# Performance work log

Hardware: AMD Instinct MI355X
Metric: run time of the kernel (lower is better)

The kernel has to match this reference:

```python
import jax, jax.numpy as jnp
import numpy as np

B, F_IN, HID, H, S = 256, 1024, 1024, 16, 128
TEMP = float((HID // H) ** 0.5)  # 8.0


def setup_inputs() -> dict:
    key = jax.random.key(0)
    ks = jax.random.split(key, 7)
    return {
        "x": jax.random.normal(ks[0], (B, F_IN, S), dtype=jnp.float32),
        "Wq": jax.random.normal(ks[1], (HID, F_IN), dtype=jnp.float32) * (1.0 / np.sqrt(F_IN)),
        "bq": jax.random.normal(ks[2], (HID,), dtype=jnp.float32) * 0.01,
        "Wk": jax.random.normal(ks[3], (HID, F_IN), dtype=jnp.float32) * (1.0 / np.sqrt(F_IN)),
        "bk": jax.random.normal(ks[4], (HID,), dtype=jnp.float32) * 0.01,
        "Wo": jax.random.normal(ks[5], (S,), dtype=jnp.float32) * (1.0 / np.sqrt(S)),
        "bo": jax.random.normal(ks[6], (1,), dtype=jnp.float32) * 0.01,
    }


def _to_heads(t):
    # (B, F, S) -> (B, H, S, F//H), matching reshape(B,H,F/H,S).permute(0,1,3,2)
    b, f, s = t.shape
    return t.reshape(b, H, f // H, s).transpose(0, 1, 3, 2)


def reference(x, Wq, bq, Wk, bk, Wo, bo):
    # 1x1 Conv1d == per-position linear over channel dim
    q = jnp.einsum('bis,hi->bhs', x, Wq) + bq[None, :, None]
    k = jnp.einsum('bis,hi->bhs', x, Wk) + bk[None, :, None]
    qh = _to_heads(q)          # (B,H,S,HID/H)
    kh = _to_heads(k)          # (B,H,S,HID/H)
    vh = _to_heads(x)          # (B,H,S,F_IN/H)  -- v is the raw input, unprojected
    scores = jnp.einsum('bhsd,bhtd->bhst', qh, kh) / TEMP
    attn = jax.nn.softmax(scores, axis=-1)
    out = jnp.einsum('bhst,bhtd->bhsd', attn, vh)   # (B,H,S,F_IN/H)
    # _reshape_from_batches: (B,H,S,dv) -> (B, F_IN, S)
    out = out.transpose(0, 1, 3, 2).reshape(x.shape[0], F_IN, S)
    # map_o: Linear(num_users, 1) over last axis, then squeeze
    score = jnp.einsum('bfs,s->bf', out, Wo) + bo[0]
    return score
```

## Files before the change

kernel.cpp:

```cpp
#include <hip/hip_runtime.h>

#define F 1024
#define S 128
#define H 16
#define D 64
#define CK 64
#define NCHUNK 16

typedef short bf16x8 __attribute__((ext_vector_type(8)));
typedef float f32x4  __attribute__((ext_vector_type(4)));

#define XS_UNITS ((size_t)256 * NCHUNK * 1024)
#define WB_UNITS ((size_t)16 * NCHUNK * 1024)
#define WS_NEED ((XS_UNITS + WB_UNITS) * 16)

struct SmemT {
    uint4 mat[2048];
    float wpart[4][S];
    float wfin[S];
};

__device__ __forceinline__ unsigned short f2bf(float f) {
    unsigned u = __float_as_uint(f);
    u += 0x7fffu + ((u >> 16) & 1u);
    return (unsigned short)(u >> 16);
}

__device__ __forceinline__ uint4 pack8(const float* f) {
    uint4 u;
    u.x = (unsigned)f2bf(f[0]) | ((unsigned)f2bf(f[1]) << 16);
    u.y = (unsigned)f2bf(f[2]) | ((unsigned)f2bf(f[3]) << 16);
    u.z = (unsigned)f2bf(f[4]) | ((unsigned)f2bf(f[5]) << 16);
    u.w = (unsigned)f2bf(f[6]) | ((unsigned)f2bf(f[7]) << 16);
    return u;
}

typedef __attribute__((address_space(1))) const unsigned int as1_u32;
typedef __attribute__((address_space(3))) unsigned int as3_u32;

__device__ __forceinline__ void async_cp16(const uint4* g, uint4* l) {
    __builtin_amdgcn_global_load_lds((as1_u32*)g, (as3_u32*)l, 16, 0, 0);
}

__global__ void prep(const float* __restrict__ x,
                     const float* __restrict__ Wq,
                     const float* __restrict__ Wk,
                     uint4* __restrict__ xs,
                     uint4* __restrict__ wb)
{
    __shared__ float tile[64 * 129];
    const int tid = threadIdx.x;
    const int blk = blockIdx.x;
    if (blk < 4096) {
        const int b = blk >> 4, ch = blk & 15;
        const float4* src = (const float4*)(x + ((size_t)b * F + ch * CK) * S);
        float4 v[8];
#pragma unroll
        for (int j = 0; j < 8; ++j) v[j] = src[tid + j * 256];
#pragma unroll
        for (int j = 0; j < 8; ++j) {
            const int e4 = tid + j * 256;
            const int i  = e4 >> 5;
            const int sc = (e4 & 31) * 4;
            tile[i * 129 + sc + 0] = v[j].x;
            tile[i * 129 + sc + 1] = v[j].y;
            tile[i * 129 + sc + 2] = v[j].z;
            tile[i * 129 + sc + 3] = v[j].w;
        }
        __syncthreads();
#pragma unroll
        for (int j = 0; j < 4; ++j) {
            const int u   = tid + j * 256;
            const int s   = u >> 3;
            const int kc  = (u & 7) ^ (s & 7);
            float f[8];
#pragma unroll
            for (int jj = 0; jj < 8; ++jj) f[jj] = tile[(kc * 8 + jj) * 129 + s];
            xs[((size_t)(b * NCHUNK + ch)) * 1024 + u] = pack8(f);
        }
    } else {
        const int blk2 = blk - 4096;
        const int h = blk2 >> 4, ch = blk2 & 15;
#pragma unroll
        for (int j = 0; j < 4; ++j) {
            const int u   = tid + j * 256;
            const int row = u >> 3;
            const int kc  = (u & 7) ^ (row & 7);
            const float* src = (row < 64)
                ? (Wq + (size_t)(h * D + row) * F + ch * CK + kc * 8)
                : (Wk + (size_t)(h * D + row - 64) * F + ch * CK + kc * 8);
            float f[8];
            float4 a = ((const float4*)src)[0];
            float4 c = ((const float4*)src)[1];
            f[0] = a.x; f[1] = a.y; f[2] = a.z; f[3] = a.w;
            f[4] = c.x; f[5] = c.y; f[6] = c.z; f[7] = c.w;
            wb[((size_t)(h * NCHUNK + ch)) * 1024 + u] = pack8(f);
        }
    }
}

__launch_bounds__(256, 4)
__global__ void attn_main(const float* __restrict__ x,
                          const uint4* __restrict__ xs,
                          const uint4* __restrict__ wb,
                          const float* __restrict__ bq,
                          const float* __restrict__ bk,
                          const float* __restrict__ Wo,
                          const float* __restrict__ bo,
                          float* __restrict__ out)
{
    __shared__ SmemT sm;
    const int tid  = threadIdx.x;
    const int lane = tid & 63;
    const int wv   = tid >> 6;
    const int l15  = lane & 15;
    const int q    = lane >> 4;

    const int g    = blockIdx.x;
    const int xcd  = g & 7;
    const int slot = g >> 3;
    const int hg   = slot >> 7;
    const int r0   = slot & 127;
    const int b    = xcd * 32 + (r0 >> 2);
    const int h    = hg * 4 + (r0 & 3);

    const float* xb = x + (size_t)b * (F * S);
    const uint4* xc = xs + ((size_t)b * NCHUNK) * 1024;
    const uint4* wc = wb + ((size_t)h * NCHUNK) * 1024;

    const int m0 = (wv & 1) * 64;
    const int n0 = (wv >> 1) * 64;

    f32x4 acc[4][4];
#pragma unroll
    for (int mt = 0; mt < 4; ++mt)
#pragma unroll
        for (int nt = 0; nt < 4; ++nt) acc[mt][nt] = (f32x4){0.f, 0.f, 0.f, 0.f};

    for (int ch = 0; ch < NCHUNK; ++ch) {
        __syncthreads();
        const uint4* wg = wc + ch * 1024 + wv * 256;
        const uint4* xg = xc + ch * 1024 + wv * 256;
#pragma unroll
        for (int k = 0; k < 4; ++k)
            async_cp16(wg + k * 64 + lane, &sm.mat[wv * 256 + k * 64]);
#pragma unroll
        for (int k = 0; k < 4; ++k)
            async_cp16(xg + k * 64 + lane, &sm.mat[1024 + wv * 256 + k * 64]);
        __syncthreads();
#pragma unroll
        for (int ks = 0; ks < 2; ++ks) {
            bf16x8 af[4], br[4];
#pragma unroll
            for (int mt = 0; mt < 4; ++mt) {
                const int row = m0 + mt * 16 + l15;
                af[mt] = *(const bf16x8*)&sm.mat[row * 8 + ((ks * 4 + q) ^ (row & 7))];
            }
#pragma unroll
            for (int nt = 0; nt < 4; ++nt) {
                const int row = n0 + nt * 16 + l15;
                br[nt] = *(const bf16x8*)&sm.mat[1024 + row * 8 + ((ks * 4 + q) ^ (row & 7))];
            }
#pragma unroll
            for (int mt = 0; mt < 4; ++mt)
#pragma unroll
                for (int nt = 0; nt < 4; ++nt)
                    acc[mt][nt] = __builtin_amdgcn_mfma_f32_16x16x32_bf16(
                        af[mt], br[nt], acc[mt][nt], 0, 0, 0);
        }
    }

    __syncthreads();
    {
        unsigned short* m16 = (unsigned short*)sm.mat;
#pragma unroll
        for (int mt = 0; mt < 4; ++mt) {
#pragma unroll
            for (int rr = 0; rr < 4; ++rr) {
                const int m = m0 + mt * 16 + q * 4 + rr;
                const int d = m & 63;
                const float bias = (m < 64) ? bq[h * D + d] : bk[h * D + d];
                const int base = (m < 64) ? 0 : 8192;
#pragma unroll
                for (int nt = 0; nt < 4; ++nt) {
                    const int s = n0 + nt * 16 + l15;
                    const float v = acc[mt][nt][rr] + bias;
                    const int unit = s * 8 + (((d >> 3)) ^ (s & 7));
                    m16[base + unit * 8 + (d & 7)] = f2bf(v);
                }
            }
        }
    }
    __syncthreads();

    f32x4 p[2][8];
#pragma unroll
    for (int mt = 0; mt < 2; ++mt)
#pragma unroll
        for (int nt = 0; nt < 8; ++nt) p[mt][nt] = (f32x4){0.f, 0.f, 0.f, 0.f};

#pragma unroll
    for (int ks = 0; ks < 2; ++ks) {
        bf16x8 a2[2], b2[8];
#pragma unroll
        for (int mt = 0; mt < 2; ++mt) {
            const int row = wv * 32 + mt * 16 + l15;
            a2[mt] = *(const bf16x8*)&sm.mat[row * 8 + ((ks * 4 + q) ^ (row & 7))];
        }
#pragma unroll
        for (int nt = 0; nt < 8; ++nt) {
            const int row = nt * 16 + l15;
            b2[nt] = *(const bf16x8*)&sm.mat[1024 + row * 8 + ((ks * 4 + q) ^ (row & 7))];
        }
#pragma unroll
        for (int mt = 0; mt < 2; ++mt)
#pragma unroll
            for (int nt = 0; nt < 8; ++nt)
                p[mt][nt] = __builtin_amdgcn_mfma_f32_16x16x32_bf16(a2[mt], b2[nt], p[mt][nt], 0, 0, 0);
    }

    float pw[8];
#pragma unroll
    for (int nt = 0; nt < 8; ++nt) pw[nt] = 0.f;

#pragma unroll
    for (int mt = 0; mt < 2; ++mt) {
#pragma unroll
        for (int rr = 0; rr < 4; ++rr) {
            const int srow = wv * 32 + mt * 16 + q * 4 + rr;
            float mx = p[mt][0][rr];
#pragma unroll
            for (int nt = 1; nt < 8; ++nt) mx = fmaxf(mx, p[mt][nt][rr]);
#pragma unroll
            for (int off = 1; off < 16; off <<= 1) mx = fmaxf(mx, __shfl_xor(mx, off));
            float e[8];
            float l = 0.f;
#pragma unroll
            for (int nt = 0; nt < 8; ++nt) {
                e[nt] = __expf((p[mt][nt][rr] - mx) * 0.125f);
                l += e[nt];
            }
#pragma unroll
            for (int off = 1; off < 16; off <<= 1) l += __shfl_xor(l, off);
            const float c = Wo[srow] / l;
#pragma unroll
            for (int nt = 0; nt < 8; ++nt) pw[nt] = fmaf(c, e[nt], pw[nt]);
        }
    }
#pragma unroll
    for (int nt = 0; nt < 8; ++nt) {
        pw[nt] += __shfl_xor(pw[nt], 16);
        pw[nt] += __shfl_xor(pw[nt], 32);
    }
    if (q == 0) {
#pragma unroll
        for (int nt = 0; nt < 8; ++nt) sm.wpart[wv][nt * 16 + l15] = pw[nt];
    }
    __syncthreads();
    if (tid < S)
        sm.wfin[tid] = sm.wpart[0][tid] + sm.wpart[1][tid] + sm.wpart[2][tid] + sm.wpart[3][tid];
    __syncthreads();

    {
        const int dd   = tid >> 2;
        const int part = tid & 3;
        const float* xv = xb + (size_t)(h * D + dd) * S + part * 32;
        float a5 = 0.f;
#pragma unroll 8
        for (int t = 0; t < 32; ++t) a5 = fmaf(sm.wfin[part * 32 + t], xv[t], a5);
        a5 += __shfl_xor(a5, 1);
        a5 += __shfl_xor(a5, 2);
        if (part == 0) out[(size_t)b * F + h * D + dd] = a5 + bo[0];
    }
}

__launch_bounds__(256, 4)
__global__ void attn_fallback(const float* __restrict__ x,
                              const float* __restrict__ Wq,
                              const float* __restrict__ bq,
                              const float* __restrict__ Wk,
                              const float* __restrict__ bk,
                              const float* __restrict__ Wo,
                              const float* __restrict__ bo,
                              float* __restrict__ out)
{
    __shared__ SmemT sm;
    const int tid  = threadIdx.x;
    const int lane = tid & 63;
    const int wv   = tid >> 6;
    const int l15  = lane & 15;
    const int q    = lane >> 4;

    const int g    = blockIdx.x;
    const int xcd  = g & 7;
    const int slot = g >> 3;
    const int hg   = slot >> 7;
    const int r0   = slot & 127;
    const int b    = xcd * 32 + (r0 >> 2);
    const int h    = hg * 4 + (r0 & 3);

    const float* xb  = x  + (size_t)b * (F * S);
    const float* wqh = Wq + (size_t)h * D * F;
    const float* wkh = Wk + (size_t)h * D * F;

    const int m0 = (wv & 1) * 64;
    const int n0 = (wv >> 1) * 64;

    f32x4 acc[4][4];
#pragma unroll
    for (int mt = 0; mt < 4; ++mt)
#pragma unroll
        for (int nt = 0; nt < 4; ++nt) acc[mt][nt] = (f32x4){0.f, 0.f, 0.f, 0.f};

    const int mq  = tid >> 2;
    const int kq  = tid & 3;
    const int s0x = (tid & 63) * 2;
    const int iq  = tid >> 6;

    for (int ch = 0; ch < NCHUNK; ++ch) {
        const int c0 = ch * CK;
        __syncthreads();
        {
            const int key = mq & 7;
            float f[16];
            const float4* srcq = (const float4*)(wqh + (size_t)mq * F + (c0 + kq * 16));
#pragma unroll
            for (int j = 0; j < 4; ++j) {
                float4 v = srcq[j];
                f[4*j] = v.x; f[4*j+1] = v.y; f[4*j+2] = v.z; f[4*j+3] = v.w;
            }
            sm.mat[mq * 8 + ((kq * 2    ) ^ key)] = pack8(f);
            sm.mat[mq * 8 + ((kq * 2 + 1) ^ key)] = pack8(f + 8);
            const float4* srck = (const float4*)(wkh + (size_t)mq * F + (c0 + kq * 16));
#pragma unroll
            for (int j = 0; j < 4; ++j) {
                float4 v = srck[j];
                f[4*j] = v.x; f[4*j+1] = v.y; f[4*j+2] = v.z; f[4*j+3] = v.w;
            }
            sm.mat[(64 + mq) * 8 + ((kq * 2    ) ^ key)] = pack8(f);
            sm.mat[(64 + mq) * 8 + ((kq * 2 + 1) ^ key)] = pack8(f + 8);
        }
        {
            const float* src = xb + (size_t)(c0 + iq * 16) * S + s0x;
            float fa[8], fb[8];
#pragma unroll
            for (int grp = 0; grp < 2; ++grp) {
#pragma unroll
                for (int j = 0; j < 8; ++j) {
                    float2 v = *(const float2*)(src + (size_t)(grp * 8 + j) * S);
                    fa[j] = v.x; fb[j] = v.y;
                }
                const int kc = iq * 2 + grp;
                sm.mat[1024 + (s0x    ) * 8 + (kc ^ ((s0x    ) & 7))] = pack8(fa);
                sm.mat[1024 + (s0x + 1) * 8 + (kc ^ ((s0x + 1) & 7))] = pack8(fb);
            }
        }
        __syncthreads();
#pragma unroll
        for (int ks = 0; ks < 2; ++ks) {
            bf16x8 af[4], br[4];
#pragma unroll
            for (int mt = 0; mt < 4; ++mt) {
                const int row = m0 + mt * 16 + l15;
                af[mt] = *(const bf16x8*)&sm.mat[row * 8 + ((ks * 4 + q) ^ (row & 7))];
            }
#pragma unroll
            for (int nt = 0; nt < 4; ++nt) {
                const int row = n0 + nt * 16 + l15;
                br[nt] = *(const bf16x8*)&sm.mat[1024 + row * 8 + ((ks * 4 + q) ^ (row & 7))];
            }
#pragma unroll
            for (int mt = 0; mt < 4; ++mt)
#pragma unroll
                for (int nt = 0; nt < 4; ++nt)
                    acc[mt][nt] = __builtin_amdgcn_mfma_f32_16x16x32_bf16(
                        af[mt], br[nt], acc[mt][nt], 0, 0, 0);
        }
    }

    __syncthreads();
    {
        unsigned short* m16 = (unsigned short*)sm.mat;
#pragma unroll
        for (int mt = 0; mt < 4; ++mt) {
#pragma unroll
            for (int rr = 0; rr < 4; ++rr) {
                const int m = m0 + mt * 16 + q * 4 + rr;
                const int d = m & 63;
                const float bias = (m < 64) ? bq[h * D + d] : bk[h * D + d];
                const int base = (m < 64) ? 0 : 8192;
#pragma unroll
                for (int nt = 0; nt < 4; ++nt) {
                    const int s = n0 + nt * 16 + l15;
                    const float v = acc[mt][nt][rr] + bias;
                    const int unit = s * 8 + (((d >> 3)) ^ (s & 7));
                    m16[base + unit * 8 + (d & 7)] = f2bf(v);
                }
            }
        }
    }
    __syncthreads();

    f32x4 p[2][8];
#pragma unroll
    for (int mt = 0; mt < 2; ++mt)
#pragma unroll
        for (int nt = 0; nt < 8; ++nt) p[mt][nt] = (f32x4){0.f, 0.f, 0.f, 0.f};

#pragma unroll
    for (int ks = 0; ks < 2; ++ks) {
        bf16x8 a2[2], b2[8];
#pragma unroll
        for (int mt = 0; mt < 2; ++mt) {
            const int row = wv * 32 + mt * 16 + l15;
            a2[mt] = *(const bf16x8*)&sm.mat[row * 8 + ((ks * 4 + q) ^ (row & 7))];
        }
#pragma unroll
        for (int nt = 0; nt < 8; ++nt) {
            const int row = nt * 16 + l15;
            b2[nt] = *(const bf16x8*)&sm.mat[1024 + row * 8 + ((ks * 4 + q) ^ (row & 7))];
        }
#pragma unroll
        for (int mt = 0; mt < 2; ++mt)
#pragma unroll
            for (int nt = 0; nt < 8; ++nt)
                p[mt][nt] = __builtin_amdgcn_mfma_f32_16x16x32_bf16(a2[mt], b2[nt], p[mt][nt], 0, 0, 0);
    }

    float pw[8];
#pragma unroll
    for (int nt = 0; nt < 8; ++nt) pw[nt] = 0.f;

#pragma unroll
    for (int mt = 0; mt < 2; ++mt) {
#pragma unroll
        for (int rr = 0; rr < 4; ++rr) {
            const int srow = wv * 32 + mt * 16 + q * 4 + rr;
            float mx = p[mt][0][rr];
#pragma unroll
            for (int nt = 1; nt < 8; ++nt) mx = fmaxf(mx, p[mt][nt][rr]);
#pragma unroll
            for (int off = 1; off < 16; off <<= 1) mx = fmaxf(mx, __shfl_xor(mx, off));
            float e[8];
            float l = 0.f;
#pragma unroll
            for (int nt = 0; nt < 8; ++nt) {
                e[nt] = __expf((p[mt][nt][rr] - mx) * 0.125f);
                l += e[nt];
            }
#pragma unroll
            for (int off = 1; off < 16; off <<= 1) l += __shfl_xor(l, off);
            const float c = Wo[srow] / l;
#pragma unroll
            for (int nt = 0; nt < 8; ++nt) pw[nt] = fmaf(c, e[nt], pw[nt]);
        }
    }
#pragma unroll
    for (int nt = 0; nt < 8; ++nt) {
        pw[nt] += __shfl_xor(pw[nt], 16);
        pw[nt] += __shfl_xor(pw[nt], 32);
    }
    if (q == 0) {
#pragma unroll
        for (int nt = 0; nt < 8; ++nt) sm.wpart[wv][nt * 16 + l15] = pw[nt];
    }
    __syncthreads();
    if (tid < S)
        sm.wfin[tid] = sm.wpart[0][tid] + sm.wpart[1][tid] + sm.wpart[2][tid] + sm.wpart[3][tid];
    __syncthreads();

    {
        const int dd   = tid >> 2;
        const int part = tid & 3;
        const float* xv = xb + (size_t)(h * D + dd) * S + part * 32;
        float a5 = 0.f;
#pragma unroll 8
        for (int t = 0; t < 32; ++t) a5 = fmaf(sm.wfin[part * 32 + t], xv[t], a5);
        a5 += __shfl_xor(a5, 1);
        a5 += __shfl_xor(a5, 2);
        if (part == 0) out[(size_t)b * F + h * D + dd] = a5 + bo[0];
    }
}

extern "C" void kernel_launch(void* const* d_in, const int* in_sizes, int n_in,
                              void* d_out, int out_size, void* d_ws, size_t ws_size,
                              hipStream_t stream) {
    const float* x  = (const float*)d_in[0];
    const float* Wq = (const float*)d_in[1];
    const float* bq = (const float*)d_in[2];
    const float* Wk = (const float*)d_in[3];
    const float* bk = (const float*)d_in[4];
    const float* Wo = (const float*)d_in[5];
    const float* bo = (const float*)d_in[6];
    float* out = (float*)d_out;

    if (ws_size >= WS_NEED) {
        uint4* xs = (uint4*)d_ws;
        uint4* wbp = (uint4*)((char*)d_ws + XS_UNITS * 16);
        prep<<<dim3(4096 + 256), dim3(256), 0, stream>>>(x, Wq, Wk, xs, wbp);
        attn_main<<<dim3(256 * H), dim3(256), 0, stream>>>(x, xs, wbp, bq, bk, Wo, bo, out);
    } else {
        attn_fallback<<<dim3(256 * H), dim3(256), 0, stream>>>(x, Wq, bq, Wk, bk, Wo, bo, out);
    }
}
```

Baseline: 379.2 us.

## Tile main GEMM over two batches and two heads with double-buffered async LDS pipeline

Each block of attn_main now computes a 256x256 projection tile covering two heads' Q/K weights and two batches' inputs, so every staged chunk is reused across both pairs. The prep layout is changed to interleave pairs of batches and heads. Chunk loads are double-buffered with global_load_lds and overlapped with MFMA work through explicit vmcnt waits, barriers and setprio. It uses 512-thread blocks and about 136 KB of dynamic LDS, which lowers occupancy. The attention and output stages then loop over the four (batch, head) combinations serially inside the block.

Result: no change. 372.1 us (-1.9%).

```diff
diff --git a/kernel.cpp b/kernel.cpp
--- a/kernel.cpp
+++ b/kernel.cpp
@@ -10,15 +10,11 @@
 typedef short bf16x8 __attribute__((ext_vector_type(8)));
 typedef float f32x4  __attribute__((ext_vector_type(4)));
 
-#define XS_UNITS ((size_t)256 * NCHUNK * 1024)
-#define WB_UNITS ((size_t)16 * NCHUNK * 1024)
+#define XS_UNITS ((size_t)128 * NCHUNK * 2048)
+#define WB_UNITS ((size_t)8 * NCHUNK * 2048)
 #define WS_NEED ((XS_UNITS + WB_UNITS) * 16)
 
-struct SmemT {
-    uint4 mat[2048];
-    float wpart[4][S];
-    float wfin[S];
-};
+#define MAIN_LDS_BYTES (8192 * 16 + 8 * 128 * 4 + 128 * 4)
 
 __device__ __forceinline__ unsigned short f2bf(float f) {
     unsigned u = __float_as_uint(f);
@@ -40,6 +36,15 @@
 
 __device__ __forceinline__ void async_cp16(const uint4* g, uint4* l) {
     __builtin_amdgcn_global_load_lds((as1_u32*)g, (as3_u32*)l, 16, 0, 0);
+}
+
+__device__ __forceinline__ void bar()   { asm volatile("s_barrier" ::: "memory"); }
+__device__ __forceinline__ void lgkm0() { asm volatile("s_waitcnt lgkmcnt(0)" ::: "memory"); }
+
+template<int N> __device__ __forceinline__ void vmcnt_wait() {
+    if constexpr (N == 8)      asm volatile("s_waitcnt vmcnt(8)" ::: "memory");
+    else if constexpr (N == 4) asm volatile("s_waitcnt vmcnt(4)" ::: "memory");
+    else                       asm volatile("s_waitcnt vmcnt(0)" ::: "memory");
 }
 
 __global__ void prep(const float* __restrict__ x,
@@ -68,38 +73,103 @@
             tile[i * 129 + sc + 3] = v[j].w;
         }
         __syncthreads();
+        uint4* dst = xs + ((size_t)(b >> 1) * NCHUNK + ch) * 2048 + (b & 1) * 128;
 #pragma unroll
         for (int j = 0; j < 4; ++j) {
-            const int u   = tid + j * 256;
-            const int s   = u >> 3;
-            const int kc  = (u & 7) ^ (s & 7);
+            const int u  = tid + j * 256;
+            const int kc = u >> 7;
+            const int s  = u & 127;
             float f[8];
 #pragma unroll
             for (int jj = 0; jj < 8; ++jj) f[jj] = tile[(kc * 8 + jj) * 129 + s];
-            xs[((size_t)(b * NCHUNK + ch)) * 1024 + u] = pack8(f);
+            dst[kc * 256 + s] = pack8(f);
         }
     } else {
         const int blk2 = blk - 4096;
         const int h = blk2 >> 4, ch = blk2 & 15;
+        uint4* dst = wb + ((size_t)(h >> 1) * NCHUNK + ch) * 2048 + (h & 1) * 128;
 #pragma unroll
         for (int j = 0; j < 4; ++j) {
-            const int u   = tid + j * 256;
-            const int row = u >> 3;
-            const int kc  = (u & 7) ^ (row & 7);
-            const float* src = (row < 64)
-                ? (Wq + (size_t)(h * D + row) * F + ch * CK + kc * 8)
-                : (Wk + (size_t)(h * D + row - 64) * F + ch * CK + kc * 8);
+            const int u  = tid + j * 256;
+            const int kc = u >> 7;
+            const int m  = u & 127;
+            const float* srcp = (m < 64)
+                ? (Wq + (size_t)(h * D + m) * F + ch * CK + kc * 8)
+                : (Wk + (size_t)(h * D + m - 64) * F + ch * CK + kc * 8);
             float f[8];
-            float4 a = ((const float4*)src)[0];
-            float4 c = ((const float4*)src)[1];
+            float4 a = ((const float4*)srcp)[0];
+            float4 c = ((const float4*)srcp)[1];
             f[0] = a.x; f[1] = a.y; f[2] = a.z; f[3] = a.w;
             f[4] = c.x; f[5] = c.y; f[6] = c.z; f[7] = c.w;
-            wb[((size_t)(h * NCHUNK + ch)) * 1024 + u] = pack8(f);
-        }
-    }
-}
-
-__launch_bounds__(256, 4)
+            dst[kc * 256 + m] = pack8(f);
+        }
+    }
+}
+
+__device__ __forceinline__ void read4(const uint4* mat, int base, bf16x8 (&r)[4]) {
+    r[0] = *(const bf16x8*)&mat[base];
+    r[1] = *(const bf16x8*)&mat[base + 16];
+    r[2] = *(const bf16x8*)&mat[base + 32];
+    r[3] = *(const bf16x8*)&mat[base + 48];
+}
+
+template<int RB>
+__device__ __forceinline__ void mfma16(f32x4 (&acc)[8][4], const bf16x8 (&af)[4], const bf16x8 (&br)[4]) {
+#pragma unroll
+    for (int mt = 0; mt < 4; ++mt)
+#pragma unroll
+        for (int nt = 0; nt < 4; ++nt)
+            acc[RB + mt][nt] = __builtin_amdgcn_mfma_f32_16x16x32_bf16(af[mt], br[nt], acc[RB + mt][nt], 0, 0, 0);
+}
+
+template<int HALF>
+__device__ __forceinline__ void stage_half(uint4* mat, const uint4* wbase, const uint4* xbase,
+                                           int tgt, int wv, int lane) {
+    const int bufb = (tgt & 1) * 4096;
+    const uint4* g;
+    int l;
+    if constexpr (HALF == 0)      { g = wbase + (size_t)tgt * 2048;        l = bufb;        }
+    else if constexpr (HALF == 1) { g = xbase + (size_t)tgt * 2048;        l = bufb + 2048; }
+    else if constexpr (HALF == 2) { g = wbase + (size_t)tgt * 2048 + 1024; l = bufb + 1024; }
+    else                          { g = xbase + (size_t)tgt * 2048 + 1024; l = bufb + 3072; }
+    async_cp16(g + wv * 128 + lane,      &mat[l + wv * 128]);
+    async_cp16(g + wv * 128 + 64 + lane, &mat[l + wv * 128 + 64]);
+}
+
+template<int CUR, bool I1, bool I2, int W1, int W2, bool DW2>
+__device__ __forceinline__ void ktile(uint4* mat, const uint4* wbase, const uint4* xbase,
+                                      int t, int wv, int lane, int wm, int wn, int q, int l15,
+                                      f32x4 (&acc)[8][4])
+{
+    bf16x8 af[4], br[4];
+    const int abase = CUR * 4096 + wm * 128 + l15;
+    const int bbase = CUR * 4096 + 2048 + wn * 64 + l15;
+    const int kq = q * 256;
+    read4(mat, abase + kq, af);
+    read4(mat, bbase + kq, br);
+    if constexpr (I1) stage_half<2>(mat, wbase, xbase, t + 1, wv, lane);
+    bar(); lgkm0();
+    __builtin_amdgcn_s_setprio(1); mfma16<0>(acc, af, br); __builtin_amdgcn_s_setprio(0);
+    bar();
+    read4(mat, abase + kq + 64, af);
+    if constexpr (I1) stage_half<3>(mat, wbase, xbase, t + 1, wv, lane);
+    bar(); lgkm0();
+    __builtin_amdgcn_s_setprio(1); mfma16<4>(acc, af, br); __builtin_amdgcn_s_setprio(0);
+    vmcnt_wait<W1>(); bar();
+    read4(mat, abase + kq + 1024, af);
+    read4(mat, bbase + kq + 1024, br);
+    if constexpr (I2) stage_half<0>(mat, wbase, xbase, t + 2, wv, lane);
+    bar(); lgkm0();
+    __builtin_amdgcn_s_setprio(1); mfma16<0>(acc, af, br); __builtin_amdgcn_s_setprio(0);
+    bar();
+    read4(mat, abase + kq + 1024 + 64, af);
+    if constexpr (I2) stage_half<1>(mat, wbase, xbase, t + 2, wv, lane);
+    bar(); lgkm0();
+    __builtin_amdgcn_s_setprio(1); mfma16<4>(acc, af, br); __builtin_amdgcn_s_setprio(0);
+    if constexpr (DW2) { vmcnt_wait<W2>(); bar(); }
+}
+
+__launch_bounds__(512, 2)
 __global__ void attn_main(const float* __restrict__ x,
                           const uint4* __restrict__ xs,
                           const uint4* __restrict__ wb,
@@ -109,170 +179,173 @@
                           const float* __restrict__ bo,
                           float* __restrict__ out)
 {
-    __shared__ SmemT sm;
+    extern __shared__ char smraw[];
+    uint4* mat   = (uint4*)smraw;
+    float* wpart = (float*)(smraw + 8192 * 16);
+    float* wfin  = wpart + 8 * 128;
+
     const int tid  = threadIdx.x;
     const int lane = tid & 63;
     const int wv   = tid >> 6;
     const int l15  = lane & 15;
     const int q    = lane >> 4;
+    const int wm   = wv >> 2;
+    const int wn   = wv & 3;
 
     const int g    = blockIdx.x;
     const int xcd  = g & 7;
     const int slot = g >> 3;
-    const int hg   = slot >> 7;
-    const int r0   = slot & 127;
-    const int b    = xcd * 32 + (r0 >> 2);
-    const int h    = hg * 4 + (r0 & 3);
-
-    const float* xb = x + (size_t)b * (F * S);
-    const uint4* xc = xs + ((size_t)b * NCHUNK) * 1024;
-    const uint4* wc = wb + ((size_t)h * NCHUNK) * 1024;
-
-    const int m0 = (wv & 1) * 64;
-    const int n0 = (wv >> 1) * 64;
-
-    f32x4 acc[4][4];
-#pragma unroll
-    for (int mt = 0; mt < 4; ++mt)
-#pragma unroll
-        for (int nt = 0; nt < 4; ++nt) acc[mt][nt] = (f32x4){0.f, 0.f, 0.f, 0.f};
-
-    for (int ch = 0; ch < NCHUNK; ++ch) {
-        __syncthreads();
-        const uint4* wg = wc + ch * 1024 + wv * 256;
-        const uint4* xg = xc + ch * 1024 + wv * 256;
-#pragma unroll
-        for (int k = 0; k < 4; ++k)
-            async_cp16(wg + k * 64 + lane, &sm.mat[wv * 256 + k * 64]);
-#pragma unroll
-        for (int k = 0; k < 4; ++k)
-            async_cp16(xg + k * 64 + lane, &sm.mat[1024 + wv * 256 + k * 64]);
-        __syncthreads();
+    const int bg   = xcd * 16 + (slot & 15);
+    const int hg   = slot >> 4;
+
+    const uint4* wbase = wb + (size_t)hg * NCHUNK * 2048;
+    const uint4* xbase = xs + (size_t)bg * NCHUNK * 2048;
+
+    f32x4 acc[8][4];
+#pragma unroll
+    for (int mi = 0; mi < 8; ++mi)
+#pragma unroll
+        for (int ni = 0; ni < 4; ++ni) acc[mi][ni] = (f32x4){0.f, 0.f, 0.f, 0.f};
+
+    stage_half<0>(mat, wbase, xbase, 0, wv, lane);
+    stage_half<1>(mat, wbase, xbase, 0, wv, lane);
+    stage_half<2>(mat, wbase, xbase, 0, wv, lane);
+    stage_half<3>(mat, wbase, xbase, 0, wv, lane);
+    stage_half<0>(mat, wbase, xbase, 1, wv, lane);
+    stage_half<1>(mat, wbase, xbase, 1, wv, lane);
+    vmcnt_wait<8>();
+    bar();
+
+#pragma unroll 1
+    for (int i = 0; i < 7; ++i) {
+        ktile<0, true, true, 8, 8, true>(mat, wbase, xbase, 2 * i,     wv, lane, wm, wn, q, l15, acc);
+        ktile<1, true, true, 8, 8, true>(mat, wbase, xbase, 2 * i + 1, wv, lane, wm, wn, q, l15, acc);
+    }
+    ktile<0, true,  false, 8, 4, true >(mat, wbase, xbase, 14, wv, lane, wm, wn, q, l15, acc);
+    ktile<1, false, false, 0, 0, false>(mat, wbase, xbase, 15, wv, lane, wm, wn, q, l15, acc);
+
+    __syncthreads();
+
+    {
+        unsigned short* m16 = (unsigned short*)mat;
+        const int hglob = hg * 2 + wm;
+#pragma unroll
+        for (int rt = 0; rt < 8; ++rt) {
+            const int mh0   = rt * 16 + q * 4;
+            const int d0    = mh0 & 63;
+            const int kbase = (mh0 < 64) ? 0 : 1024;
+            float bias4[4];
+#pragma unroll
+            for (int rr = 0; rr < 4; ++rr)
+                bias4[rr] = (mh0 < 64) ? bq[hglob * D + d0 + rr] : bk[hglob * D + d0 + rr];
+#pragma unroll
+            for (int ct = 0; ct < 4; ++ct) {
+                const int col = wn * 64 + ct * 16 + l15;
+                const int bj  = col >> 7;
+                const int s   = col & 127;
+                const int c   = wm * 2 + bj;
+                unsigned long long pv = 0;
+#pragma unroll
+                for (int rr = 0; rr < 4; ++rr)
+                    pv |= (unsigned long long)f2bf(acc[rt][ct][rr] + bias4[rr]) << (16 * rr);
+                const int unit = c * 2048 + kbase + s * 8 + ((d0 >> 3) ^ (s & 7));
+                *(unsigned long long*)&m16[unit * 8 + (d0 & 7)] = pv;
+            }
+        }
+    }
+    __syncthreads();
+
+    for (int c = 0; c < 4; ++c) {
+        const int qb = c * 2048;
+        const int kb = c * 2048 + 1024;
+        f32x4 p[8];
+#pragma unroll
+        for (int nt = 0; nt < 8; ++nt) p[nt] = (f32x4){0.f, 0.f, 0.f, 0.f};
 #pragma unroll
         for (int ks = 0; ks < 2; ++ks) {
-            bf16x8 af[4], br[4];
-#pragma unroll
-            for (int mt = 0; mt < 4; ++mt) {
-                const int row = m0 + mt * 16 + l15;
-                af[mt] = *(const bf16x8*)&sm.mat[row * 8 + ((ks * 4 + q) ^ (row & 7))];
-            }
-#pragma unroll
-            for (int nt = 0; nt < 4; ++nt) {
-                const int row = n0 + nt * 16 + l15;
-                br[nt] = *(const bf16x8*)&sm.mat[1024 + row * 8 + ((ks * 4 + q) ^ (row & 7))];
-            }
-#pragma unroll
-            for (int mt = 0; mt < 4; ++mt)
-#pragma unroll
-                for (int nt = 0; nt < 4; ++nt)
-                    acc[mt][nt] = __builtin_amdgcn_mfma_f32_16x16x32_bf16(
-                        af[mt], br[nt], acc[mt][nt], 0, 0, 0);
-        }
-    }
-
-    __syncthreads();
-    {
-        unsigned short* m16 = (unsigned short*)sm.mat;
-#pragma unroll
-        for (int mt = 0; mt < 4; ++mt) {
-#pragma unroll
-            for (int rr = 0; rr < 4; ++rr) {
-                const int m = m0 + mt * 16 + q * 4 + rr;
-                const int d = m & 63;
-                const float bias = (m < 64) ? bq[h * D + d] : bk[h * D + d];
-                const int base = (m < 64) ? 0 : 8192;
-#pragma unroll
-                for (int nt = 0; nt < 4; ++nt) {
-                    const int s = n0 + nt * 16 + l15;
-                    const float v = acc[mt][nt][rr] + bias;
-                    const int unit = s * 8 + (((d >> 3)) ^ (s & 7));
-                    m16[base + unit * 8 + (d & 7)] = f2bf(v);
-                }
-            }
-        }
-    }
-    __syncthreads();
-
-    f32x4 p[2][8];
-#pragma unroll
-    for (int mt = 0; mt < 2; ++mt)
-#pragma unroll
-        for (int nt = 0; nt < 8; ++nt) p[mt][nt] = (f32x4){0.f, 0.f, 0.f, 0.f};
-
-#pragma unroll
-    for (int ks = 0; ks < 2; ++ks) {
-        bf16x8 a2[2], b2[8];
-#pragma unroll
-        for (int mt = 0; mt < 2; ++mt) {
-            const int row = wv * 32 + mt * 16 + l15;
-            a2[mt] = *(const bf16x8*)&sm.mat[row * 8 + ((ks * 4 + q) ^ (row & 7))];
-        }
-#pragma unroll
-        for (int nt = 0; nt < 8; ++nt) {
-            const int row = nt * 16 + l15;
-            b2[nt] = *(const bf16x8*)&sm.mat[1024 + row * 8 + ((ks * 4 + q) ^ (row & 7))];
-        }
-#pragma unroll
-        for (int mt = 0; mt < 2; ++mt)
+            const int kcq  = ks * 4 + q;
+            const int arow = wv * 16 + l15;
+            bf16x8 a2 = *(const bf16x8*)&mat[qb + arow * 8 + (kcq ^ (arow & 7))];
+            bf16x8 b2[8];
+#pragma unroll
+            for (int nt = 0; nt < 8; ++nt) {
+                const int trow = nt * 16 + l15;
+                b2[nt] = *(const bf16x8*)&mat[kb + trow * 8 + (kcq ^ (trow & 7))];
+            }
 #pragma unroll
             for (int nt = 0; nt < 8; ++nt)
-                p[mt][nt] = __builtin_amdgcn_mfma_f32_16x16x32_bf16(a2[mt], b2[nt], p[mt][nt], 0, 0, 0);
-    }
-
-    float pw[8];
-#pragma unroll
-    for (int nt = 0; nt < 8; ++nt) pw[nt] = 0.f;
-
-#pragma unroll
-    for (int mt = 0; mt < 2; ++mt) {
+                p[nt] = __builtin_amdgcn_mfma_f32_16x16x32_bf16(a2, b2[nt], p[nt], 0, 0, 0);
+        }
+        float pw[8];
+#pragma unroll
+        for (int nt = 0; nt < 8; ++nt) pw[nt] = 0.f;
 #pragma unroll
         for (int rr = 0; rr < 4; ++rr) {
-            const int srow = wv * 32 + mt * 16 + q * 4 + rr;
-            float mx = p[mt][0][rr];
-#pragma unroll
-            for (int nt = 1; nt < 8; ++nt) mx = fmaxf(mx, p[mt][nt][rr]);
+            const int srow = wv * 16 + q * 4 + rr;
+            float mx = p[0][rr];
+#pragma unroll
+            for (int nt = 1; nt < 8; ++nt) mx = fmaxf(mx, p[nt][rr]);
 #pragma unroll
             for (int off = 1; off < 16; off <<= 1) mx = fmaxf(mx, __shfl_xor(mx, off));
             float e[8];
             float l = 0.f;
 #pragma unroll
             for (int nt = 0; nt < 8; ++nt) {
-                e[nt] = __expf((p[mt][nt][rr] - mx) * 0.125f);
+                e[nt] = __expf((p[nt][rr] - mx) * 0.125f);
                 l += e[nt];
             }
 #pragma unroll
             for (int off = 1; off < 16; off <<= 1) l += __shfl_xor(l, off);
-            const float c = Wo[srow] / l;
-#pragma unroll
-            for (int nt = 0; nt < 8; ++nt) pw[nt] = fmaf(c, e[nt], pw[nt]);
-        }
-    }
-#pragma unroll
-    for (int nt = 0; nt < 8; ++nt) {
-        pw[nt] += __shfl_xor(pw[nt], 16);
-        pw[nt] += __shfl_xor(pw[nt], 32);
-    }
-    if (q == 0) {
-#pragma unroll
-        for (int nt = 0; nt < 8; ++nt) sm.wpart[wv][nt * 16 + l15] = pw[nt];
-    }
-    __syncthreads();
-    if (tid < S)
-        sm.wfin[tid] = sm.wpart[0][tid] + sm.wpart[1][tid] + sm.wpart[2][tid] + sm.wpart[3][tid];
-    __syncthreads();
-
-    {
-        const int dd   = tid >> 2;
-        const int part = tid & 3;
-        const float* xv = xb + (size_t)(h * D + dd) * S + part * 32;
-        float a5 = 0.f;
-#pragma unroll 8
-        for (int t = 0; t < 32; ++t) a5 = fmaf(sm.wfin[part * 32 + t], xv[t], a5);
-        a5 += __shfl_xor(a5, 1);
-        a5 += __shfl_xor(a5, 2);
-        if (part == 0) out[(size_t)b * F + h * D + dd] = a5 + bo[0];
-    }
-}
+            const float cw = Wo[srow] / l;
+#pragma unroll
+            for (int nt = 0; nt < 8; ++nt) pw[nt] = fmaf(cw, e[nt], pw[nt]);
+        }
+#pragma unroll
+        for (int nt = 0; nt < 8; ++nt) {
+            pw[nt] += __shfl_xor(pw[nt], 16);
+            pw[nt] += __shfl_xor(pw[nt], 32);
+        }
+        if (q == 0) {
+#pragma unroll
+            for (int nt = 0; nt < 8; ++nt) wpart[wv * 128 + nt * 16 + l15] = pw[nt];
+        }
+        __syncthreads();
+        if (tid < 128) {
+            float sum = 0.f;
+#pragma unroll
+            for (int w = 0; w < 8; ++w) sum += wpart[w * 128 + tid];
+            wfin[tid] = sum;
+        }
+        __syncthreads();
+        {
+            const int bglob = bg * 2 + (c & 1);
+            const int hglob = hg * 2 + (c >> 1);
+            const int dd = tid >> 3, part = tid & 7;
+            const float4* xv = (const float4*)(x + (size_t)bglob * (F * S)
+                                                 + (size_t)(hglob * D + dd) * S + part * 16);
+            float a5 = 0.f;
+#pragma unroll
+            for (int j = 0; j < 4; ++j) {
+                float4 vv = xv[j];
+                a5 = fmaf(wfin[part * 16 + j * 4 + 0], vv.x, a5);
+                a5 = fmaf(wfin[part * 16 + j * 4 + 1], vv.y, a5);
+                a5 = fmaf(wfin[part * 16 + j * 4 + 2], vv.z, a5);
+                a5 = fmaf(wfin[part * 16 + j * 4 + 3], vv.w, a5);
+            }
+            a5 += __shfl_xor(a5, 1);
+            a5 += __shfl_xor(a5, 2);
+            a5 += __shfl_xor(a5, 4);
+            if (part == 0) out[(size_t)bglob * F + hglob * D + dd] = a5 + bo[0];
+        }
+        __syncthreads();
+    }
+}
+
+struct SmemT {
+    uint4 mat[2048];
+    float wpart[4][S];
+    float wfin[S];
+};
 
 __launch_bounds__(256, 4)
 __global__ void attn_fallback(const float* __restrict__ x,
@@ -495,10 +568,16 @@
     float* out = (float*)d_out;
 
     if (ws_size >= WS_NEED) {
-        uint4* xs = (uint4*)d_ws;
+        uint4* xsp = (uint4*)d_ws;
         uint4* wbp = (uint4*)((char*)d_ws + XS_UNITS * 16);
-        prep<<<dim3(4096 + 256), dim3(256), 0, stream>>>(x, Wq, Wk, xs, wbp);
-        attn_main<<<dim3(256 * H), dim3(256), 0, stream>>>(x, xs, wbp, bq, bk, Wo, bo, out);
+        static bool attr_done = false;
+        if (!attr_done) {
+            (void)hipFuncSetAttribute(reinterpret_cast<const void*>(attn_main),
+                                      hipFuncAttributeMaxDynamicSharedMemorySize, MAIN_LDS_BYTES);
+            attr_done = true;
+        }
+        prep<<<dim3(4096 + 256), dim3(256), 0, stream>>>(x, Wq, Wk, xsp, wbp);
+        attn_main<<<dim3(1024), dim3(512), MAIN_LDS_BYTES, stream>>>(x, xsp, wbp, bq, bk, Wo, bo, out);
     } else {
         attn_fallback<<<dim3(256 * H), dim3(256), 0, stream>>>(x, Wq, bq, Wk, bk, Wo, bo, out);
     }
```
